# Performance work log

Measured on AMD Instinct MI355X. Metric: run time of the kernel, lower is better.

## Reference

```python
import jax, jax.numpy as jnp
import numpy as np

NUM_ITERATIONS = 3


def squash(t, axis=-1):
    # scale * t / sqrt(||t||^2 + eps), scale = ||t||^2 / (1 + ||t||^2)
    sq = jnp.sum(t * t, axis=axis, keepdims=True)
    return (sq / (1.0 + sq)) * t / jnp.sqrt(sq + 1e-8)


def setup_inputs() -> dict:
    key = jax.random.key(0)
    k1, k2 = jax.random.split(key)
    B, C, R, I, O = 128, 10, 8192, 8, 16
    x = jax.random.normal(k1, (B, R, I), dtype=jnp.float32)
    route_weights = jax.random.normal(k2, (C, R, I, O), dtype=jnp.float32) * 0.1
    return {"x": x, "route_weights": route_weights}


def reference(x, route_weights):
    # x: [B, R, I]; route_weights: [C, R, I, O]
    u_hat = jnp.einsum('bri,crio->bcro', x, route_weights)  # [B, C, R, O]
    B, C, R, O = u_hat.shape
    b_ij = jnp.zeros((B, C, R), dtype=u_hat.dtype)
    v_j = None
    for it in range(NUM_ITERATIONS):
        c_ij = jax.nn.softmax(b_ij, axis=1)                 # [B, C, R]
        s_j = jnp.einsum('bcr,bcro->bco', c_ij, u_hat)      # [B, C, O]
        v_j = squash(s_j, axis=-1)                          # [B, C, O]
        if it < NUM_ITERATIONS - 1:
            a_ij = jnp.einsum('bcro,bco->bcr', u_hat, v_j)  # [B, C, R]
            b_ij = b_ij + a_ij
    return v_j
```

## Files before the change

### kernel.cpp

```cpp
#include <hip/hip_runtime.h>
#include <hip/hip_fp16.h>
#include <math.h>

#define B_ 128
#define C_ 10
#define R_ 8192
#define I_ 8
#define O_ 16

typedef __attribute__((ext_vector_type(8))) _Float16 half8;
typedef __attribute__((ext_vector_type(16))) float f32x16;

#define WROW 64
#define WZERO 80
#define SBO (C_ * B_ * O_)
#define NRED 32

__device__ __forceinline__ unsigned pk2(float a, float b) {
    __half2 h = __floats2half2_rn(a, b);
    return *(unsigned*)&h;
}

__global__ __launch_bounds__(256, 5) void fused_iter(const float* __restrict__ x,
                                                     const float* __restrict__ w,
                                                     const float* __restrict__ vsum,
                                                     __half* __restrict__ part,
                                                     int mode) {
    __shared__ unsigned wls[(80 + 1) * WROW];

    const int tid = threadIdx.x;
    const int wave = tid >> 6;
    const int lane = tid & 63;
    const int n = lane & 31;
    const int g = lane >> 5;
    const int rp_m = (lane & 31) >> 4;
    const int o_m = lane & 15;
    const int b = wave * 32 + n;
    const int r0 = blockIdx.x * 8;

#pragma unroll
    for (int k = 0; k < 5; ++k) {
        const int id = k * 256 + tid;
        const int o = id & 15;
        const int r = (id >> 4) & 7;
        const int c = id >> 7;
        const float* wp = w + ((size_t)(c * R_ + r0 + r) * 8) * 16 + o;
        const float f0 = wp[0],  f1 = wp[16],  f2 = wp[32],  f3 = wp[48];
        const float f4 = wp[64], f5 = wp[80],  f6 = wp[96],  f7 = wp[112];
        *(uint4*)(wls + (c * 8 + r) * WROW + o * 4) =
            make_uint4(pk2(f0, f1), pk2(f2, f3), pk2(f4, f5), pk2(f6, f7));
    }
    if (tid < WROW) wls[WZERO * WROW + tid] = 0u;

    union H8 { uint4 u; half8 h; };
    half8 xbr[4];
#pragma unroll
    for (int rp = 0; rp < 4; ++rp) {
        const int row = 2 * rp + g;
        const float* xp = x + ((size_t)b * R_ + r0 + row) * 8;
        const float4 v0 = *(const float4*)xp;
        const float4 v1 = *(const float4*)(xp + 4);
        H8 t;
        t.u = make_uint4(pk2(v0.x, v0.y), pk2(v0.z, v0.w),
                         pk2(v1.x, v1.y), pk2(v1.z, v1.w));
        xbr[rp] = t.h;
    }

    __syncthreads();

    const int act = (g == rp_m);

    if (mode) {
        float dinv[4];
        {
            float dacc[4] = {0.f, 0.f, 0.f, 0.f};
#pragma unroll 1
            for (int c = 0; c < C_; ++c) {
                const float4* vp = (const float4*)(vsum + ((size_t)c * B_ + b) * O_ + 4 * g);
                const float4 va = vp[0];
                const float4 vb = vp[2];
#pragma unroll
                for (int rp = 0; rp < 4; ++rp) {
                    const int woff = act ? ((c * 8 + 2 * rp + g) * WROW + o_m * 4)
                                         : (WZERO * WROW);
                    const half8 a = *(const half8*)(wls + woff);
                    f32x16 u;
#pragma unroll
                    for (int j = 0; j < 16; ++j) u[j] = 0.f;
                    u = __builtin_amdgcn_mfma_f32_32x32x16_f16(a, xbr[rp], u, 0, 0, 0);
                    const float p0 = u[0] * va.x + u[1] * va.y + u[2] * va.z + u[3] * va.w
                                   + u[4] * vb.x + u[5] * vb.y + u[6] * vb.z + u[7] * vb.w;
                    const float p1 = u[8] * va.x + u[9] * va.y + u[10] * va.z + u[11] * va.w
                                   + u[12] * vb.x + u[13] * vb.y + u[14] * vb.z + u[15] * vb.w;
                    const float send = g ? p0 : p1;
                    const float recv = __shfl_xor(send, 32);
                    const float pg = (g ? p1 : p0) + recv;
                    dacc[rp] += __expf(pg);
                }
            }
#pragma unroll
            for (int rp = 0; rp < 4; ++rp) dinv[rp] = 1.0f / dacc[rp];
        }

#pragma unroll 1
        for (int c = 0; c < C_; ++c) {
            const float4* vp = (const float4*)(vsum + ((size_t)c * B_ + b) * O_ + 4 * g);
            const float4 va = vp[0];
            const float4 vb = vp[2];
            float acc[8];
#pragma unroll
            for (int rp = 0; rp < 4; ++rp) {
                const int woff = act ? ((c * 8 + 2 * rp + g) * WROW + o_m * 4)
                                     : (WZERO * WROW);
                const half8 a = *(const half8*)(wls + woff);
                f32x16 u;
#pragma unroll
                for (int j = 0; j < 16; ++j) u[j] = 0.f;
                u = __builtin_amdgcn_mfma_f32_32x32x16_f16(a, xbr[rp], u, 0, 0, 0);
                const float p0 = u[0] * va.x + u[1] * va.y + u[2] * va.z + u[3] * va.w
                               + u[4] * vb.x + u[5] * vb.y + u[6] * vb.z + u[7] * vb.w;
                const float p1 = u[8] * va.x + u[9] * va.y + u[10] * va.z + u[11] * va.w
                               + u[12] * vb.x + u[13] * vb.y + u[14] * vb.z + u[15] * vb.w;
                const float send = g ? p0 : p1;
                const float recv = __shfl_xor(send, 32);
                const float pg = (g ? p1 : p0) + recv;
                const float w_own = __expf(pg) * dinv[rp];
                const float w_oth = __shfl_xor(w_own, 32);
                const float c0 = g ? w_oth : w_own;
                const float c1 = g ? w_own : w_oth;
                if (rp == 0) {
#pragma unroll
                    for (int j = 0; j < 8; ++j) acc[j] = c0 * u[j] + c1 * u[j + 8];
                } else {
#pragma unroll
                    for (int j = 0; j < 8; ++j) acc[j] += c0 * u[j] + c1 * u[j + 8];
                }
            }
            __half* pp = part + (((size_t)blockIdx.x * C_ + c) * B_ + b) * O_;
            *(uint2*)(pp + 4 * g)     = make_uint2(pk2(acc[0], acc[1]), pk2(acc[2], acc[3]));
            *(uint2*)(pp + 8 + 4 * g) = make_uint2(pk2(acc[4], acc[5]), pk2(acc[6], acc[7]));
        }
    } else {
#pragma unroll 1
        for (int c = 0; c < C_; ++c) {
            f32x16 acc;
#pragma unroll
            for (int j = 0; j < 16; ++j) acc[j] = 0.f;
#pragma unroll
            for (int rp = 0; rp < 4; ++rp) {
                const int woff = act ? ((c * 8 + 2 * rp + g) * WROW + o_m * 4)
                                     : (WZERO * WROW);
                const half8 a = *(const half8*)(wls + woff);
                acc = __builtin_amdgcn_mfma_f32_32x32x16_f16(a, xbr[rp], acc, 0, 0, 0);
            }
            const float f0 = (acc[0] + acc[8])  * 0.1f, f1 = (acc[1] + acc[9])  * 0.1f;
            const float f2 = (acc[2] + acc[10]) * 0.1f, f3 = (acc[3] + acc[11]) * 0.1f;
            const float f4 = (acc[4] + acc[12]) * 0.1f, f5 = (acc[5] + acc[13]) * 0.1f;
            const float f6 = (acc[6] + acc[14]) * 0.1f, f7 = (acc[7] + acc[15]) * 0.1f;
            __half* pp = part + (((size_t)blockIdx.x * C_ + c) * B_ + b) * O_;
            *(uint2*)(pp + 4 * g)     = make_uint2(pk2(f0, f1), pk2(f2, f3));
            *(uint2*)(pp + 8 + 4 * g) = make_uint2(pk2(f4, f5), pk2(f6, f7));
        }
    }
}

__global__ __launch_bounds__(256) void reduce1(const __half* __restrict__ part,
                                               float* __restrict__ part2) {
    const int t8 = blockIdx.x * 256 + threadIdx.x;
    const __half* p = part + (size_t)(blockIdx.y * NRED) * SBO + (size_t)t8 * 8;
    float s0 = 0.f, s1 = 0.f, s2 = 0.f, s3 = 0.f;
    float s4 = 0.f, s5 = 0.f, s6 = 0.f, s7 = 0.f;
#pragma unroll 8
    for (int s = 0; s < NRED; ++s) {
        const uint4 v = *(const uint4*)(p + (size_t)s * SBO);
        const float2 f0 = __half22float2(*(const __half2*)&v.x);
        const float2 f1 = __half22float2(*(const __half2*)&v.y);
        const float2 f2 = __half22float2(*(const __half2*)&v.z);
        const float2 f3 = __half22float2(*(const __half2*)&v.w);
        s0 += f0.x; s1 += f0.y; s2 += f1.x; s3 += f1.y;
        s4 += f2.x; s5 += f2.y; s6 += f3.x; s7 += f3.y;
    }
    float* q = part2 + (size_t)blockIdx.y * SBO + (size_t)t8 * 8;
    *(float4*)q       = make_float4(s0, s1, s2, s3);
    *(float4*)(q + 4) = make_float4(s4, s5, s6, s7);
}

__global__ __launch_bounds__(256) void finish_pass(const float* __restrict__ part2,
                                                   float* __restrict__ vsum,
                                                   float* __restrict__ out,
                                                   int mode) {
    const int t = blockIdx.x * 256 + threadIdx.x;
    float sum = 0.f;
#pragma unroll
    for (int s = 0; s < 1024 / NRED; ++s)
        sum += part2[(size_t)s * SBO + t];

    float sq = sum * sum;
    sq += __shfl_xor(sq, 1);
    sq += __shfl_xor(sq, 2);
    sq += __shfl_xor(sq, 4);
    sq += __shfl_xor(sq, 8);
    const float scale = sq / ((1.0f + sq) * sqrtf(sq + 1e-8f));
    const float v = scale * sum;

    if (mode == 0) {
        vsum[t] = v;
    } else if (mode == 1) {
        vsum[t] += v;
    } else {
        const int o = t & 15, b = (t >> 4) & 127, c = t >> 11;
        out[((size_t)b * C_ + c) * O_ + o] = v;
    }
}

extern "C" void kernel_launch(void* const* d_in, const int* in_sizes, int n_in,
                              void* d_out, int out_size, void* d_ws, size_t ws_size,
                              hipStream_t stream) {
    const float* x = (const float*)d_in[0];
    const float* w = (const float*)d_in[1];
    float* out = (float*)d_out;

    __half* part = (__half*)d_ws;
    float* part2 = (float*)(part + (size_t)1024 * SBO);
    float* vsum  = part2 + (size_t)32 * SBO;

    const dim3 fgrid(R_ / 8);
    const dim3 rgrid(10, 1024 / NRED);
    const dim3 ggrid(80);

    fused_iter<<<fgrid, 256, 0, stream>>>(x, w, vsum, part, 0);
    reduce1<<<rgrid, 256, 0, stream>>>(part, part2);
    finish_pass<<<ggrid, 256, 0, stream>>>(part2, vsum, out, 0);

    fused_iter<<<fgrid, 256, 0, stream>>>(x, w, vsum, part, 1);
    reduce1<<<rgrid, 256, 0, stream>>>(part, part2);
    finish_pass<<<ggrid, 256, 0, stream>>>(part2, vsum, out, 1);

    fused_iter<<<fgrid, 256, 0, stream>>>(x, w, vsum, part, 1);
    reduce1<<<rgrid, 256, 0, stream>>>(part, part2);
    finish_pass<<<ggrid, 256, 0, stream>>>(part2, vsum, out, 2);
}
```

Baseline: 233.0 us.

## Stage x through swizzled LDS and halve rows per block when workspace allows

Loads x cooperatively with coalesced float4 reads into a swizzled LDS tile instead of per-lane strided global reads, then gathers the MFMA B operands from LDS. The kernel is templated on rows per block, and when the workspace is large enough it uses 4 rows per block, which doubles the grid and the number of partial slots. This aims at better load coalescing and more parallelism, at the cost of twice the partial-sum traffic for the reduction kernels and extra LDS use per block.

```diff
diff --git a/kernel.cpp b/kernel.cpp
--- a/kernel.cpp
+++ b/kernel.cpp
@@ -11,22 +11,26 @@
 typedef __attribute__((ext_vector_type(8))) _Float16 half8;
 typedef __attribute__((ext_vector_type(16))) float f32x16;
 
+#define XROW 512
 #define WROW 64
-#define WZERO 80
 #define SBO (C_ * B_ * O_)
-#define NRED 32
 
 __device__ __forceinline__ unsigned pk2(float a, float b) {
     __half2 h = __floats2half2_rn(a, b);
     return *(unsigned*)&h;
 }
 
-__global__ __launch_bounds__(256, 5) void fused_iter(const float* __restrict__ x,
-                                                     const float* __restrict__ w,
-                                                     const float* __restrict__ vsum,
-                                                     __half* __restrict__ part,
-                                                     int mode) {
-    __shared__ unsigned wls[(80 + 1) * WROW];
+template<int TR, int MINW>
+__global__ __launch_bounds__(256, MINW) void fused_iter(const float* __restrict__ x,
+                                                        const float* __restrict__ w,
+                                                        const float* __restrict__ vsum,
+                                                        __half* __restrict__ part,
+                                                        int mode) {
+    constexpr int RP = TR / 2;
+    constexpr int WR = C_ * TR;
+    constexpr int LOG2TR = (TR == 8) ? 3 : 2;
+    __shared__ unsigned xls[TR * XROW];
+    __shared__ unsigned wls[(WR + 1) * WROW];
 
     const int tid = threadIdx.x;
     const int wave = tid >> 6;
@@ -36,53 +40,60 @@
     const int rp_m = (lane & 31) >> 4;
     const int o_m = lane & 15;
     const int b = wave * 32 + n;
-    const int r0 = blockIdx.x * 8;
-
-#pragma unroll
-    for (int k = 0; k < 5; ++k) {
+    const int r0 = blockIdx.x * TR;
+
+#pragma unroll
+    for (int k = 0; k < TR; ++k) {
+        const int f = k * 256 + tid;
+        const int q = f & 1;
+        const int rr = (f >> 1) & (TR - 1);
+        const int bb = f >> (1 + LOG2TR);
+        const float4 v = *(const float4*)(x + ((size_t)bb * R_ + r0 + rr) * 8 + q * 4);
+        *(uint2*)(xls + rr * XROW + ((bb * 4 + q * 2) ^ (rr << 2))) =
+            make_uint2(pk2(v.x, v.y), pk2(v.z, v.w));
+    }
+    constexpr int NW = WR * 16;
+#pragma unroll
+    for (int k = 0; k < (NW + 255) / 256; ++k) {
         const int id = k * 256 + tid;
-        const int o = id & 15;
-        const int r = (id >> 4) & 7;
-        const int c = id >> 7;
-        const float* wp = w + ((size_t)(c * R_ + r0 + r) * 8) * 16 + o;
-        const float f0 = wp[0],  f1 = wp[16],  f2 = wp[32],  f3 = wp[48];
-        const float f4 = wp[64], f5 = wp[80],  f6 = wp[96],  f7 = wp[112];
-        *(uint4*)(wls + (c * 8 + r) * WROW + o * 4) =
-            make_uint4(pk2(f0, f1), pk2(f2, f3), pk2(f4, f5), pk2(f6, f7));
-    }
-    if (tid < WROW) wls[WZERO * WROW + tid] = 0u;
-
-    union H8 { uint4 u; half8 h; };
-    half8 xbr[4];
-#pragma unroll
-    for (int rp = 0; rp < 4; ++rp) {
+        if ((NW & 255) == 0 || id < NW) {
+            const int o = id & 15;
+            const int r = (id >> 4) & (TR - 1);
+            const int c = id >> (4 + LOG2TR);
+            const float* wp = w + ((size_t)(c * R_ + r0 + r) * 8) * 16 + o;
+            const float f0 = wp[0],  f1 = wp[16],  f2 = wp[32],  f3 = wp[48];
+            const float f4 = wp[64], f5 = wp[80],  f6 = wp[96],  f7 = wp[112];
+            *(uint4*)(wls + (c * TR + r) * WROW + o * 4) =
+                make_uint4(pk2(f0, f1), pk2(f2, f3), pk2(f4, f5), pk2(f6, f7));
+        }
+    }
+    if (tid < WROW) wls[WR * WROW + tid] = 0u;
+    __syncthreads();
+
+    const int act = (g == rp_m);
+
+    half8 xbr[RP];
+#pragma unroll
+    for (int rp = 0; rp < RP; ++rp) {
         const int row = 2 * rp + g;
-        const float* xp = x + ((size_t)b * R_ + r0 + row) * 8;
-        const float4 v0 = *(const float4*)xp;
-        const float4 v1 = *(const float4*)(xp + 4);
-        H8 t;
-        t.u = make_uint4(pk2(v0.x, v0.y), pk2(v0.z, v0.w),
-                         pk2(v1.x, v1.y), pk2(v1.z, v1.w));
-        xbr[rp] = t.h;
-    }
-
-    __syncthreads();
-
-    const int act = (g == rp_m);
+        xbr[rp] = *(const half8*)(xls + row * XROW + ((b * 4) ^ (row << 2)));
+    }
 
     if (mode) {
-        float dinv[4];
+        float dinv[RP];
         {
-            float dacc[4] = {0.f, 0.f, 0.f, 0.f};
+            float dacc[RP];
+#pragma unroll
+            for (int rp = 0; rp < RP; ++rp) dacc[rp] = 0.f;
 #pragma unroll 1
             for (int c = 0; c < C_; ++c) {
                 const float4* vp = (const float4*)(vsum + ((size_t)c * B_ + b) * O_ + 4 * g);
                 const float4 va = vp[0];
                 const float4 vb = vp[2];
 #pragma unroll
-                for (int rp = 0; rp < 4; ++rp) {
-                    const int woff = act ? ((c * 8 + 2 * rp + g) * WROW + o_m * 4)
-                                         : (WZERO * WROW);
+                for (int rp = 0; rp < RP; ++rp) {
+                    const int woff = act ? ((c * TR + 2 * rp + g) * WROW + o_m * 4)
+                                         : (WR * WROW);
                     const half8 a = *(const half8*)(wls + woff);
                     f32x16 u;
 #pragma unroll
@@ -99,7 +110,7 @@
                 }
             }
 #pragma unroll
-            for (int rp = 0; rp < 4; ++rp) dinv[rp] = 1.0f / dacc[rp];
+            for (int rp = 0; rp < RP; ++rp) dinv[rp] = 1.0f / dacc[rp];
         }
 
 #pragma unroll 1
@@ -109,9 +120,9 @@
             const float4 vb = vp[2];
             float acc[8];
 #pragma unroll
-            for (int rp = 0; rp < 4; ++rp) {
-                const int woff = act ? ((c * 8 + 2 * rp + g) * WROW + o_m * 4)
-                                     : (WZERO * WROW);
+            for (int rp = 0; rp < RP; ++rp) {
+                const int woff = act ? ((c * TR + 2 * rp + g) * WROW + o_m * 4)
+                                     : (WR * WROW);
                 const half8 a = *(const half8*)(wls + woff);
                 f32x16 u;
 #pragma unroll
@@ -147,9 +158,9 @@
 #pragma unroll
             for (int j = 0; j < 16; ++j) acc[j] = 0.f;
 #pragma unroll
-            for (int rp = 0; rp < 4; ++rp) {
-                const int woff = act ? ((c * 8 + 2 * rp + g) * WROW + o_m * 4)
-                                     : (WZERO * WROW);
+            for (int rp = 0; rp < RP; ++rp) {
+                const int woff = act ? ((c * TR + 2 * rp + g) * WROW + o_m * 4)
+                                     : (WR * WROW);
                 const half8 a = *(const half8*)(wls + woff);
                 acc = __builtin_amdgcn_mfma_f32_32x32x16_f16(a, xbr[rp], acc, 0, 0, 0);
             }
@@ -167,11 +178,11 @@
 __global__ __launch_bounds__(256) void reduce1(const __half* __restrict__ part,
                                                float* __restrict__ part2) {
     const int t8 = blockIdx.x * 256 + threadIdx.x;
-    const __half* p = part + (size_t)(blockIdx.y * NRED) * SBO + (size_t)t8 * 8;
+    const __half* p = part + (size_t)(blockIdx.y * 32) * SBO + (size_t)t8 * 8;
     float s0 = 0.f, s1 = 0.f, s2 = 0.f, s3 = 0.f;
     float s4 = 0.f, s5 = 0.f, s6 = 0.f, s7 = 0.f;
 #pragma unroll 8
-    for (int s = 0; s < NRED; ++s) {
+    for (int s = 0; s < 32; ++s) {
         const uint4 v = *(const uint4*)(p + (size_t)s * SBO);
         const float2 f0 = __half22float2(*(const __half2*)&v.x);
         const float2 f1 = __half22float2(*(const __half2*)&v.y);
@@ -188,11 +199,11 @@
 __global__ __launch_bounds__(256) void finish_pass(const float* __restrict__ part2,
                                                    float* __restrict__ vsum,
                                                    float* __restrict__ out,
-                                                   int mode) {
+                                                   int mode, int ngroups) {
     const int t = blockIdx.x * 256 + threadIdx.x;
     float sum = 0.f;
-#pragma unroll
-    for (int s = 0; s < 1024 / NRED; ++s)
+#pragma unroll 8
+    for (int s = 0; s < ngroups; ++s)
         sum += part2[(size_t)s * SBO + t];
 
     float sq = sum * sum;
@@ -220,23 +231,27 @@
     const float* w = (const float*)d_in[1];
     float* out = (float*)d_out;
 
+    const size_t need4 = (size_t)(R_ / 4) * SBO * 2
+                       + (size_t)64 * SBO * 4
+                       + (size_t)SBO * 4;
+    const bool use4 = (ws_size >= need4);
+    const int slots = use4 ? (R_ / 4) : (R_ / 8);
+    const int groups = slots / 32;
+
     __half* part = (__half*)d_ws;
-    float* part2 = (float*)(part + (size_t)1024 * SBO);
-    float* vsum  = part2 + (size_t)32 * SBO;
-
-    const dim3 fgrid(R_ / 8);
-    const dim3 rgrid(10, 1024 / NRED);
+    float* part2 = (float*)(part + (size_t)slots * SBO);
+    float* vsum  = part2 + (size_t)groups * SBO;
+
+    const dim3 fgrid(slots);
+    const dim3 rgrid(10, groups);
     const dim3 ggrid(80);
 
-    fused_iter<<<fgrid, 256, 0, stream>>>(x, w, vsum, part, 0);
-    reduce1<<<rgrid, 256, 0, stream>>>(part, part2);
-    finish_pass<<<ggrid, 256, 0, stream>>>(part2, vsum, out, 0);
-
-    fused_iter<<<fgrid, 256, 0, stream>>>(x, w, vsum, part, 1);
-    reduce1<<<rgrid, 256, 0, stream>>>(part, part2);
-    finish_pass<<<ggrid, 256, 0, stream>>>(part2, vsum, out, 1);
-
-    fused_iter<<<fgrid, 256, 0, stream>>>(x, w, vsum, part, 1);
-    reduce1<<<rgrid, 256, 0, stream>>>(part, part2);
-    finish_pass<<<ggrid, 256, 0, stream>>>(part2, vsum, out, 2);
-}
+    for (int it = 0; it < 3; ++it) {
+        const int mode = (it > 0);
+        const int fmode = (it == 2) ? 2 : it;
+        if (use4) fused_iter<4, 5><<<fgrid, 256, 0, stream>>>(x, w, vsum, part, mode);
+        else      fused_iter<8, 4><<<fgrid, 256, 0, stream>>>(x, w, vsum, part, mode);
+        reduce1<<<rgrid, 256, 0, stream>>>(part, part2);
+        finish_pass<<<ggrid, 256, 0, stream>>>(part2, vsum, out, fmode, groups);
+    }
+}
```

Result: slower. 267.3 us (+14.7%).

## Process two row-groups per block and pre-reduce partials in LDS

Applied to the files above, without the earlier changes.

Blocks grow to 512 threads, with each half handling 8 rows, so there are half as many blocks. x is now staged through swizzled shared memory for coalesced loads. The two halves' partial sums are added in LDS before being written to global, which halves the partial buffer and the downstream reduction traffic. The cost is extra __syncthreads inside the class loop, plus higher LDS use and register pressure per block.

```diff
diff --git a/kernel.cpp b/kernel.cpp
--- a/kernel.cpp
+++ b/kernel.cpp
@@ -11,64 +11,108 @@
 typedef __attribute__((ext_vector_type(8))) _Float16 half8;
 typedef __attribute__((ext_vector_type(16))) float f32x16;
 
+#define XROW 512
 #define WROW 64
 #define WZERO 80
 #define SBO (C_ * B_ * O_)
-#define NRED 32
+#define SLOTS 512
+#define NRED 8
 
 __device__ __forceinline__ unsigned pk2(float a, float b) {
     __half2 h = __floats2half2_rn(a, b);
     return *(unsigned*)&h;
 }
 
-__global__ __launch_bounds__(256, 5) void fused_iter(const float* __restrict__ x,
+__global__ __launch_bounds__(512, 4) void fused_iter(const float* __restrict__ x,
                                                      const float* __restrict__ w,
                                                      const float* __restrict__ vsum,
                                                      __half* __restrict__ part,
                                                      int mode) {
-    __shared__ unsigned wls[(80 + 1) * WROW];
-
-    const int tid = threadIdx.x;
+    __shared__ unsigned xls[2 * 8 * XROW];
+    __shared__ unsigned wls[2 * 81 * WROW];
+
+    const int tid  = threadIdx.x;
     const int wave = tid >> 6;
+    const int sg   = wave >> 2;
+    const int stid = tid & 255;
     const int lane = tid & 63;
-    const int n = lane & 31;
-    const int g = lane >> 5;
+    const int n    = lane & 31;
+    const int g    = lane >> 5;
     const int rp_m = (lane & 31) >> 4;
-    const int o_m = lane & 15;
-    const int b = wave * 32 + n;
-    const int r0 = blockIdx.x * 8;
-
+    const int o_m  = lane & 15;
+    const int b    = (wave & 3) * 32 + n;
+    const int r0   = blockIdx.x * 16 + sg * 8;
+
+    unsigned* const xbase = xls + sg * (8 * XROW);
+    unsigned* const wbase = wls + sg * (81 * WROW);
+    unsigned* const red_u = xls;
+
+#pragma unroll
+    for (int k = 0; k < 8; ++k) {
+        const int f = k * 256 + stid;
+        const int bb = f >> 4;
+        const int rr = (f >> 1) & 7;
+        const int q = f & 1;
+        const float4 v = *(const float4*)(x + ((size_t)bb * R_ + r0 + rr) * 8 + q * 4);
+        *(uint2*)(xbase + rr * XROW + ((bb * 4 + q * 2) ^ (rr << 2))) =
+            make_uint2(pk2(v.x, v.y), pk2(v.z, v.w));
+    }
 #pragma unroll
     for (int k = 0; k < 5; ++k) {
-        const int id = k * 256 + tid;
+        const int id = k * 256 + stid;
         const int o = id & 15;
         const int r = (id >> 4) & 7;
         const int c = id >> 7;
         const float* wp = w + ((size_t)(c * R_ + r0 + r) * 8) * 16 + o;
         const float f0 = wp[0],  f1 = wp[16],  f2 = wp[32],  f3 = wp[48];
         const float f4 = wp[64], f5 = wp[80],  f6 = wp[96],  f7 = wp[112];
-        *(uint4*)(wls + (c * 8 + r) * WROW + o * 4) =
+        *(uint4*)(wbase + (c * 8 + r) * WROW + o * 4) =
             make_uint4(pk2(f0, f1), pk2(f2, f3), pk2(f4, f5), pk2(f6, f7));
     }
-    if (tid < WROW) wls[WZERO * WROW + tid] = 0u;
-
-    union H8 { uint4 u; half8 h; };
+    if (stid < WROW) wbase[WZERO * WROW + stid] = 0u;
+    __syncthreads();
+
+    const int act = (g == rp_m);
+
     half8 xbr[4];
 #pragma unroll
     for (int rp = 0; rp < 4; ++rp) {
         const int row = 2 * rp + g;
-        const float* xp = x + ((size_t)b * R_ + r0 + row) * 8;
-        const float4 v0 = *(const float4*)xp;
-        const float4 v1 = *(const float4*)(xp + 4);
-        H8 t;
-        t.u = make_uint4(pk2(v0.x, v0.y), pk2(v0.z, v0.w),
-                         pk2(v1.x, v1.y), pk2(v1.z, v1.w));
-        xbr[rp] = t.h;
-    }
-
+        xbr[rp] = *(const half8*)(xbase + row * XROW + ((b * 4) ^ (row << 2)));
+    }
     __syncthreads();
 
-    const int act = (g == rp_m);
+#define RED_WRITE_AND_FLUSH(A0,A1,A2,A3,A4,A5,A6,A7)                           \
+    {                                                                          \
+        const int cp = c & 1;                                                  \
+        unsigned* rw = red_u + ((cp * 2 + sg) * 128 + b) * 10;                 \
+        *(uint2*)(rw + 2 * g)     = make_uint2(pk2(A0, A1), pk2(A2, A3));      \
+        *(uint2*)(rw + 4 + 2 * g) = make_uint2(pk2(A4, A5), pk2(A6, A7));      \
+        if (cp == 1) {                                                         \
+            __syncthreads();                                                   \
+            const int cp2 = tid >> 8, t2 = tid & 255;                          \
+            const int b2 = t2 >> 1, oh = t2 & 1;                               \
+            const int cout = c - 1 + cp2;                                      \
+            const unsigned* r0p = red_u + ((cp2 * 2 + 0) * 128 + b2) * 10 + oh * 4; \
+            const unsigned* r1p = red_u + ((cp2 * 2 + 1) * 128 + b2) * 10 + oh * 4; \
+            const uint2 xa = *(const uint2*)r0p;                               \
+            const uint2 xb2 = *(const uint2*)(r0p + 2);                        \
+            const uint2 ya = *(const uint2*)r1p;                               \
+            const uint2 yb = *(const uint2*)(r1p + 2);                         \
+            unsigned ua[4] = {xa.x, xa.y, xb2.x, xb2.y};                       \
+            unsigned ub[4] = {ya.x, ya.y, yb.x, yb.y};                         \
+            unsigned uo[4];                                                    \
+            _Pragma("unroll")                                                  \
+            for (int j = 0; j < 4; ++j) {                                      \
+                const float2 fa = __half22float2(*(const __half2*)&ua[j]);     \
+                const float2 fb = __half22float2(*(const __half2*)&ub[j]);     \
+                uo[j] = pk2(fa.x + fb.x, fa.y + fb.y);                         \
+            }                                                                  \
+            *(uint4*)(part + ((size_t)blockIdx.x * C_ + cout) * (B_ * O_)      \
+                      + b2 * O_ + oh * 8) = make_uint4(uo[0], uo[1], uo[2], uo[3]); \
+            __syncthreads();                                                   \
+        }                                                                      \
+    }
 
     if (mode) {
         float dinv[4];
@@ -83,7 +127,7 @@
                 for (int rp = 0; rp < 4; ++rp) {
                     const int woff = act ? ((c * 8 + 2 * rp + g) * WROW + o_m * 4)
                                          : (WZERO * WROW);
-                    const half8 a = *(const half8*)(wls + woff);
+                    const half8 a = *(const half8*)(wbase + woff);
                     f32x16 u;
 #pragma unroll
                     for (int j = 0; j < 16; ++j) u[j] = 0.f;
@@ -112,7 +156,7 @@
             for (int rp = 0; rp < 4; ++rp) {
                 const int woff = act ? ((c * 8 + 2 * rp + g) * WROW + o_m * 4)
                                      : (WZERO * WROW);
-                const half8 a = *(const half8*)(wls + woff);
+                const half8 a = *(const half8*)(wbase + woff);
                 f32x16 u;
 #pragma unroll
                 for (int j = 0; j < 16; ++j) u[j] = 0.f;
@@ -136,9 +180,8 @@
                     for (int j = 0; j < 8; ++j) acc[j] += c0 * u[j] + c1 * u[j + 8];
                 }
             }
-            __half* pp = part + (((size_t)blockIdx.x * C_ + c) * B_ + b) * O_;
-            *(uint2*)(pp + 4 * g)     = make_uint2(pk2(acc[0], acc[1]), pk2(acc[2], acc[3]));
-            *(uint2*)(pp + 8 + 4 * g) = make_uint2(pk2(acc[4], acc[5]), pk2(acc[6], acc[7]));
+            RED_WRITE_AND_FLUSH(acc[0], acc[1], acc[2], acc[3],
+                                acc[4], acc[5], acc[6], acc[7]);
         }
     } else {
 #pragma unroll 1
@@ -150,18 +193,17 @@
             for (int rp = 0; rp < 4; ++rp) {
                 const int woff = act ? ((c * 8 + 2 * rp + g) * WROW + o_m * 4)
                                      : (WZERO * WROW);
-                const half8 a = *(const half8*)(wls + woff);
+                const half8 a = *(const half8*)(wbase + woff);
                 acc = __builtin_amdgcn_mfma_f32_32x32x16_f16(a, xbr[rp], acc, 0, 0, 0);
             }
             const float f0 = (acc[0] + acc[8])  * 0.1f, f1 = (acc[1] + acc[9])  * 0.1f;
             const float f2 = (acc[2] + acc[10]) * 0.1f, f3 = (acc[3] + acc[11]) * 0.1f;
             const float f4 = (acc[4] + acc[12]) * 0.1f, f5 = (acc[5] + acc[13]) * 0.1f;
             const float f6 = (acc[6] + acc[14]) * 0.1f, f7 = (acc[7] + acc[15]) * 0.1f;
-            __half* pp = part + (((size_t)blockIdx.x * C_ + c) * B_ + b) * O_;
-            *(uint2*)(pp + 4 * g)     = make_uint2(pk2(f0, f1), pk2(f2, f3));
-            *(uint2*)(pp + 8 + 4 * g) = make_uint2(pk2(f4, f5), pk2(f6, f7));
+            RED_WRITE_AND_FLUSH(f0, f1, f2, f3, f4, f5, f6, f7);
         }
     }
+#undef RED_WRITE_AND_FLUSH
 }
 
 __global__ __launch_bounds__(256) void reduce1(const __half* __restrict__ part,
@@ -170,7 +212,7 @@
     const __half* p = part + (size_t)(blockIdx.y * NRED) * SBO + (size_t)t8 * 8;
     float s0 = 0.f, s1 = 0.f, s2 = 0.f, s3 = 0.f;
     float s4 = 0.f, s5 = 0.f, s6 = 0.f, s7 = 0.f;
-#pragma unroll 8
+#pragma unroll
     for (int s = 0; s < NRED; ++s) {
         const uint4 v = *(const uint4*)(p + (size_t)s * SBO);
         const float2 f0 = __half22float2(*(const __half2*)&v.x);
@@ -191,8 +233,8 @@
                                                    int mode) {
     const int t = blockIdx.x * 256 + threadIdx.x;
     float sum = 0.f;
-#pragma unroll
-    for (int s = 0; s < 1024 / NRED; ++s)
+#pragma unroll 8
+    for (int s = 0; s < SLOTS / NRED; ++s)
         sum += part2[(size_t)s * SBO + t];
 
     float sq = sum * sum;
@@ -221,22 +263,18 @@
     float* out = (float*)d_out;
 
     __half* part = (__half*)d_ws;
-    float* part2 = (float*)(part + (size_t)1024 * SBO);
-    float* vsum  = part2 + (size_t)32 * SBO;
-
-    const dim3 fgrid(R_ / 8);
-    const dim3 rgrid(10, 1024 / NRED);
+    float* part2 = (float*)(part + (size_t)SLOTS * SBO);
+    float* vsum  = part2 + (size_t)(SLOTS / NRED) * SBO;
+
+    const dim3 fgrid(R_ / 16);
+    const dim3 rgrid(10, SLOTS / NRED);
     const dim3 ggrid(80);
 
-    fused_iter<<<fgrid, 256, 0, stream>>>(x, w, vsum, part, 0);
-    reduce1<<<rgrid, 256, 0, stream>>>(part, part2);
-    finish_pass<<<ggrid, 256, 0, stream>>>(part2, vsum, out, 0);
-
-    fused_iter<<<fgrid, 256, 0, stream>>>(x, w, vsum, part, 1);
-    reduce1<<<rgrid, 256, 0, stream>>>(part, part2);
-    finish_pass<<<ggrid, 256, 0, stream>>>(part2, vsum, out, 1);
-
-    fused_iter<<<fgrid, 256, 0, stream>>>(x, w, vsum, part, 1);
-    reduce1<<<rgrid, 256, 0, stream>>>(part, part2);
-    finish_pass<<<ggrid, 256, 0, stream>>>(part2, vsum, out, 2);
-}
+    for (int it = 0; it < 3; ++it) {
+        const int mode = (it > 0);
+        const int fmode = (it == 2) ? 2 : it;
+        fused_iter<<<fgrid, 512, 0, stream>>>(x, w, vsum, part, mode);
+        reduce1<<<rgrid, 256, 0, stream>>>(part, part2);
+        finish_pass<<<ggrid, 256, 0, stream>>>(part2, vsum, out, fmode);
+    }
+}
```

Result: faster. 217.0 us (-6.9%).
